# Kernel tuning notes

Hardware: AMD Instinct MI355X
Metric: run time of the kernel (lower is better)

Reference implementation:

```python
import jax, jax.numpy as jnp
import numpy as np

# --- hyperparameters (match init_kwargs / torch defaults) ---
BLOCK_SIZE = 11
MAX_DISP = 48
CONF_TH = 0.3
DS = 2
ALPHA = 0.85          # photometric SSIM weight
GT_TH = 2.0           # GT anchor threshold
SIGN_W, MAG_W = 0.3, 0.7
W_GT, W_PHOTO, W_SIGNMAG, W_SMOOTH = 1.0, 1.0, 0.5, 0.1


def _avg_pool(x, k, stride, pad):
    # torch F.avg_pool2d with count_include_pad=True (default): zero-padded sum / k^2
    s = jax.lax.reduce_window(x, 0.0, jax.lax.add, (1, 1, k, k), (1, 1, stride, stride),
                              ((0, 0), (0, 0), (pad, pad), (pad, pad)))
    return s / (k * k)


def _ssim(x, y):
    C1, C2 = 0.01 ** 2, 0.03 ** 2
    p = lambda t: _avg_pool(t, 3, 1, 1)
    mx, my = p(x), p(y)
    sx = jnp.maximum(p(x * x) - mx * mx, 0.0)
    sy = jnp.maximum(p(y * y) - my * my, 0.0)
    sxy = p(x * y) - mx * my
    n = (2 * mx * my + C1) * (2 * sxy + C2)
    d = (mx * mx + my * my + C1) * (sx + sy + C2)
    return jnp.clip((1 - n / d) / 2, 0.0, 1.0)


def _gt_anchor(pred, gt, conf, occ):
    pos = (gt > GT_TH).astype(pred.dtype)
    trust = conf * occ * pos
    return (trust * jnp.abs(pred - gt)).sum() / jnp.maximum(trust.sum(), 1.0)


def _photometric(disp, left, right):
    B, C, H, W = left.shape
    xb = jnp.arange(W, dtype=disp.dtype)[None, None, None, :]
    xs = xb - disp                                   # sampling x coord (grid_sample, align_corners=True)
    xc = jnp.clip(xs, 0.0, W - 1.0)                  # padding_mode='border'
    x0 = jnp.floor(xc)
    w = xc - x0
    x0i = x0.astype(jnp.int32)
    x1i = jnp.minimum(x0i + 1, W - 1)
    gather = lambda idx: jnp.take_along_axis(right, jnp.broadcast_to(idx, (B, C, H, W)), axis=3)
    warped = gather(x0i) * (1.0 - w) + gather(x1i) * w   # y grid is identity under align_corners
    valid = ((xs > 0) & (xs < W - 1)).astype(disp.dtype)
    l1 = jnp.abs(left - warped).mean(axis=1, keepdims=True)
    ss = _ssim(left, warped).mean(axis=1, keepdims=True)
    err = ALPHA * ss + (1.0 - ALPHA) * l1
    return (err * valid).sum() / jnp.maximum(valid.sum(), 1.0)


def _compute_ncc_disp(left, right):
    B, C, Ho, Wo = left.shape
    lg = _avg_pool(left, DS, DS, 0).mean(axis=1, keepdims=True)   # half-res grayscale
    rg = _avg_pool(right, DS, DS, 0).mean(axis=1, keepdims=True)
    H, W = lg.shape[2], lg.shape[3]
    md = MAX_DISP // DS
    bs, pad = BLOCK_SIZE, BLOCK_SIZE // 2
    p = lambda t: _avg_pool(t, bs, 1, pad)
    lm = p(lg)
    ls = jnp.sqrt(jnp.maximum(p(lg * lg) - lm * lm, 1e-8))
    best_c = jnp.full((B, 1, H, W), -1.0, dtype=jnp.float32)
    best_d = jnp.zeros((B, 1, H, W), dtype=jnp.float32)
    for d in range(-md, md + 1):          # fixed small set of shift offsets
        if d == 0:
            continue
        if d > 0:
            rs = jnp.pad(rg[:, :, :, d:], ((0, 0), (0, 0), (0, 0), (0, d)))
        else:
            rs = jnp.pad(rg[:, :, :, :W + d], ((0, 0), (0, 0), (0, 0), (-d, 0)))
        rm = p(rs)
        rstd = jnp.sqrt(jnp.maximum(p(rs * rs) - rm * rm, 1e-8))
        cross = p(lg * rs)
        ncc = (cross - lm * rm) / (ls * rstd + 1e-8)
        better = ncc > best_c
        best_c = jnp.where(better, ncc, best_c)
        best_d = jnp.where(better, jnp.float32(d), best_d)
    nd = best_d * float(DS)
    nc = jnp.maximum(best_c, 0.0)
    # nearest upsample back to full res (exact integer factor)
    nd = jnp.repeat(jnp.repeat(nd, DS, axis=2), DS, axis=3)
    nc = jnp.repeat(jnp.repeat(nc, DS, axis=2), DS, axis=3)
    nc = nc * (nc > CONF_TH).astype(nc.dtype)
    return jax.lax.stop_gradient(nd), jax.lax.stop_gradient(nc)   # torch @no_grad


def _sign_magnitude(pred, left, right):
    nd, nc = _compute_ncc_disp(left, right)
    active = (nc > 0).astype(pred.dtype)
    n = jnp.maximum(active.sum(), 1.0)
    sign_map = jnp.sign(nd) * active
    l_sign = (jnp.maximum(-pred * sign_map, 0.0) * active).sum() / n
    l_mag = (nc * jnp.abs(pred - nd) * active).sum() / n
    return SIGN_W * l_sign + MAG_W * l_mag


def _smoothness(disp, img):
    ddx = jnp.abs(disp[:, :, :, 1:] - disp[:, :, :, :-1])
    ddy = jnp.abs(disp[:, :, 1:, :] - disp[:, :, :-1, :])
    idx = jnp.abs(img[:, :, :, 1:] - img[:, :, :, :-1]).mean(axis=1, keepdims=True)
    idy = jnp.abs(img[:, :, 1:, :] - img[:, :, :-1, :]).mean(axis=1, keepdims=True)
    return (ddx * jnp.exp(-idx)).mean() + (ddy * jnp.exp(-idy)).mean()


def _total_loss(pred, gt, conf, occ, left, right):
    return (W_GT * _gt_anchor(pred, gt, conf, occ)
            + W_PHOTO * _photometric(pred, left, right)
            + W_SIGNMAG * _sign_magnitude(pred, left, right)
            + W_SMOOTH * _smoothness(pred, left))


def setup_inputs() -> dict:
    key = jax.random.key(0)
    k = jax.random.split(key, 6)
    B, H, W = 4, 544, 960
    return {
        "pred_disp": jax.random.normal(k[0], (B, 1, H, W), dtype=jnp.float32) * 8.0,
        "gt_disp": jax.random.uniform(k[1], (B, 1, H, W), dtype=jnp.float32) * 20.0,
        "gt_conf": jax.random.uniform(k[2], (B, 1, H, W), dtype=jnp.float32),
        "gt_occ": jax.random.uniform(k[3], (B, 1, H, W), dtype=jnp.float32),
        "left_img": jax.random.uniform(k[4], (B, 3, H, W), dtype=jnp.float32),
        "right_img": jax.random.uniform(k[5], (B, 3, H, W), dtype=jnp.float32),
    }


def reference(pred_disp, gt_disp, gt_conf, gt_occ, left_img, right_img):
    return _total_loss(pred_disp, gt_disp, gt_conf, gt_occ, left_img, right_img)
```

## Files before the change

kernel.cpp:

```cpp
#include <hip/hip_runtime.h>
#include <hip/hip_bf16.h>

constexpr int B  = 4;
constexpr int H  = 544;
constexpr int W  = 960;
constexpr int H2 = 272;
constexpr int W2 = 480;
constexpr int NH = B * H2 * W2;
constexpr int NF = B * H * W;

constexpr int TPW = 32, TPH = 8;
constexpr int SW = TPW + 2, SH = TPH + 2;
constexpr int NSTAGE = SW * SH;
constexpr int GX = W / TPW;
constexpr int GY = H / TPH;
constexpr int NBLK  = GX * GY * B;
constexpr int NBLK2 = (NH + 255) / 256;

__device__ inline float waveSum(float v) {
  #pragma unroll
  for (int off = 32; off > 0; off >>= 1) v += __shfl_down(v, off, 64);
  return v;
}

__global__ __launch_bounds__(256) void k_pix(const float* __restrict__ pred,
                                             const float* __restrict__ gt,
                                             const float* __restrict__ conf,
                                             const float* __restrict__ occ,
                                             const float* __restrict__ left,
                                             const float* __restrict__ right,
                                             float* __restrict__ lg,
                                             float* __restrict__ rg,
                                             float* __restrict__ partialsA) {
  const int bx = blockIdx.x % GX;
  const int by = (blockIdx.x / GX) % GY;
  const int b  = blockIdx.x / (GX * GY);
  const int x0 = bx * TPW, y0 = by * TPH;
  const int tid = threadIdx.x;

  const float* dispb = pred + (size_t)b * H * W;
  const float* lb = left  + (size_t)b * 3 * H * W;
  const float* rb = right + (size_t)b * 3 * H * W;

  __shared__ float4 L4s[NSTAGE];
  __shared__ float4 W4s[NSTAGE];

  for (int e = tid; e < NSTAGE; e += 256) {
    int r = e / SW, c = e % SW;
    int yy = y0 - 1 + r, xx = x0 - 1 + c;
    float4 l4 = make_float4(0.f, 0.f, 0.f, 0.f);
    float4 w4 = make_float4(0.f, 0.f, 0.f, 0.f);
    if (yy >= 0 && yy < H && xx >= 0 && xx < W) {
      float dv = dispb[yy * W + xx];
      float xsv = (float)xx - dv;
      float xc = fminf(fmaxf(xsv, 0.f), (float)(W - 1));
      float x0f = floorf(xc);
      float w = xc - x0f;
      int x0i = (int)x0f;
      int x1i = min(x0i + 1, W - 1);
      const float* l0 = lb + (size_t)yy * W;
      const float* r0 = rb + (size_t)yy * W;
      l4.x = l0[xx];
      l4.y = l0[(size_t)H * W + xx];
      l4.z = l0[2 * (size_t)H * W + xx];
      l4.w = dv;
      w4.x = r0[x0i] * (1.f - w) + r0[x1i] * w;
      w4.y = r0[(size_t)H * W + x0i] * (1.f - w) + r0[(size_t)H * W + x1i] * w;
      w4.z = r0[2 * (size_t)H * W + x0i] * (1.f - w) + r0[2 * (size_t)H * W + x1i] * w;
    }
    L4s[e] = l4; W4s[e] = w4;
  }
  __syncthreads();

  if (tid < 64) {
    int hx = tid & 15, hy = tid >> 4;
    int y2g = (y0 >> 1) + hy, x2g = (x0 >> 1) + hx;
    int i00 = (2 * hy + 1) * SW + (2 * hx + 1);
    float4 a00 = L4s[i00], a01 = L4s[i00 + 1], a10 = L4s[i00 + SW], a11 = L4s[i00 + SW + 1];
    float sl = 0.f;
    sl += a00.x + a01.x + a10.x + a11.x;
    sl += a00.y + a01.y + a10.y + a11.y;
    sl += a00.z + a01.z + a10.z + a11.z;
    float sr = 0.f;
    int yy2 = y0 + 2 * hy, xx2 = x0 + 2 * hx;
    #pragma unroll
    for (int c = 0; c < 3; c++) {
      const float* rp = rb + (size_t)(c * H + yy2) * W + xx2;
      sr += rp[0] + rp[1] + rp[W] + rp[W + 1];
    }
    size_t ho = (size_t)b * (H2 * W2) + (size_t)y2g * W2 + x2g;
    lg[ho] = sl * (1.f / 12.f);
    rg[ho] = sr * (1.f / 12.f);
  }

  float v[6];
  #pragma unroll
  for (int s = 0; s < 6; s++) v[s] = 0.f;

  {
    const int tx = tid & 31, ty = tid >> 5;
    const int x = x0 + tx, y = y0 + ty;
    const size_t gidx = (size_t)b * H * W + (size_t)y * W + x;
    const int ci = (ty + 1) * SW + (tx + 1);

    float sl[3] = {0,0,0}, sw[3] = {0,0,0}, sl2[3] = {0,0,0},
          sw2[3] = {0,0,0}, slw[3] = {0,0,0};
    float4 cl4, cw4, rl4, dl4;
    #pragma unroll
    for (int dy = -1; dy <= 1; dy++) {
      #pragma unroll
      for (int dx = -1; dx <= 1; dx++) {
        int ni = ci + dy * SW + dx;
        float4 a = L4s[ni];
        float4 wv = W4s[ni];
        sl[0] += a.x;  sl2[0] += a.x * a.x;  sw[0] += wv.x;  sw2[0] += wv.x * wv.x;  slw[0] += a.x * wv.x;
        sl[1] += a.y;  sl2[1] += a.y * a.y;  sw[1] += wv.y;  sw2[1] += wv.y * wv.y;  slw[1] += a.y * wv.y;
        sl[2] += a.z;  sl2[2] += a.z * a.z;  sw[2] += wv.z;  sw2[2] += wv.z * wv.z;  slw[2] += a.z * wv.z;
        if (dy == 0 && dx == 0) { cl4 = a; cw4 = wv; }
        if (dy == 0 && dx == 1) rl4 = a;
        if (dy == 1 && dx == 0) dl4 = a;
      }
    }
    float ds = cl4.w;

    {
      float g = gt[gidx];
      float trust = (g > 2.0f) ? conf[gidx] * occ[gidx] : 0.f;
      v[0] = trust * fabsf(ds - g);
      v[1] = trust;
    }

    {
      float xs = (float)x - ds;
      bool valid = (xs > 0.f) && (xs < (float)(W - 1));
      float cl[3] = {cl4.x, cl4.y, cl4.z};
      float cw[3] = {cw4.x, cw4.y, cw4.z};
      float ssm = 0.f, l1m = 0.f;
      #pragma unroll
      for (int c = 0; c < 3; c++) {
        float mx = sl[c] * (1.f / 9.f), my = sw[c] * (1.f / 9.f);
        float sx = fmaxf(sl2[c] * (1.f / 9.f) - mx * mx, 0.f);
        float sy = fmaxf(sw2[c] * (1.f / 9.f) - my * my, 0.f);
        float sxy = slw[c] * (1.f / 9.f) - mx * my;
        float n  = (2.f * mx * my + 1e-4f) * (2.f * sxy + 9e-4f);
        float dd = (mx * mx + my * my + 1e-4f) * (sx + sy + 9e-4f);
        float ss = (1.f - n / dd) * 0.5f;
        ss = fminf(fmaxf(ss, 0.f), 1.f);
        ssm += ss;
        l1m += fabsf(cl[c] - cw[c]);
      }
      ssm *= (1.f / 3.f); l1m *= (1.f / 3.f);
      float err = 0.85f * ssm + 0.15f * l1m;
      if (valid) { v[2] = err; v[3] = 1.f; }
    }

    if (x < W - 1) {
      float ddx = fabsf(rl4.w - ds);
      float idx = fabsf(rl4.x - cl4.x) + fabsf(rl4.y - cl4.y) + fabsf(rl4.z - cl4.z);
      v[4] = ddx * __expf(-idx * (1.f / 3.f));
    }
    if (y < H - 1) {
      float ddy = fabsf(dl4.w - ds);
      float idy = fabsf(dl4.x - cl4.x) + fabsf(dl4.y - cl4.y) + fabsf(dl4.z - cl4.z);
      v[5] = ddy * __expf(-idy * (1.f / 3.f));
    }
  }

  __shared__ float sm[4][6];
  int wave = threadIdx.x >> 6, lane = threadIdx.x & 63;
  #pragma unroll
  for (int s = 0; s < 6; s++) {
    float r = waveSum(v[s]);
    if (lane == 0) sm[wave][s] = r;
  }
  __syncthreads();
  if (threadIdx.x < 6) {
    float t = sm[0][threadIdx.x] + sm[1][threadIdx.x] +
              sm[2][threadIdx.x] + sm[3][threadIdx.x];
    partialsA[(size_t)threadIdx.x * NBLK + blockIdx.x] = t;
  }
}

__global__ __launch_bounds__(256) void k_ncc(const float* __restrict__ lg,
                                             const float* __restrict__ rg,
                                             float* __restrict__ bcA,
                                             float* __restrict__ bdA) {
  const int z = blockIdx.z;
  const int b = z >> 1, grp = z & 1;
  const int dmin = grp ? 1 : -24;
  const int x0 = blockIdx.x * 64;
  const int y0 = blockIdx.y * 8;
  const int tid = threadIdx.x;

  __shared__ __align__(16) float SM[5844];
  float* LGs = SM;
  float* RMS = SM;
  float* RGs = SM + 1392;
  float* POOL = SM + 3140;
  float* P1 = SM + 5444;
  float* P2 = SM + 5644;

  const float* lgb = lg + (size_t)b * (H2 * W2);
  const float* rgb = rg + (size_t)b * (H2 * W2);

  for (int e = tid; e < 18 * 74; e += 256) {
    int r = e / 74, c = e % 74;
    int gy = y0 - 5 + r, gxx = x0 - 5 + c;
    LGs[e] = (gy >= 0 && gy < H2 && gxx >= 0 && gxx < W2) ? lgb[gy * W2 + gxx] : 0.f;
  }
  const int col0RG = x0 - 5 + dmin;
  for (int e = tid; e < 18 * 97; e += 256) {
    int r = e / 97, c = e % 97;
    int gy = y0 - 5 + r, gxx = col0RG + c;
    RGs[e] = (gy >= 0 && gy < H2 && gxx >= 0 && gxx < W2) ? rgb[gy * W2 + gxx] : 0.f;
  }
  __syncthreads();

  const int hg = tid & 7, hr = tid >> 3;
  float lgc[18];
  float* LH1 = POOL;
  float* LH2 = POOL + 1152;
  if (hr < 18) {
    #pragma unroll
    for (int k = 0; k < 18; k++) lgc[k] = LGs[hr * 74 + 8 * hg + k];
    float w1[8], w2[8];
    float s1 = 0.f, s2 = 0.f;
    #pragma unroll
    for (int k = 0; k < 11; k++) { s1 += lgc[k]; s2 += lgc[k] * lgc[k]; }
    w1[0] = s1; w2[0] = s2;
    #pragma unroll
    for (int j = 1; j < 8; j++) {
      s1 += lgc[j + 10] - lgc[j - 1];
      s2 += lgc[j + 10] * lgc[j + 10] - lgc[j - 1] * lgc[j - 1];
      w1[j] = s1; w2[j] = s2;
    }
    *(float4*)&LH1[hr * 64 + 8 * hg]     = make_float4(w1[0], w1[1], w1[2], w1[3]);
    *(float4*)&LH1[hr * 64 + 8 * hg + 4] = make_float4(w1[4], w1[5], w1[6], w1[7]);
    *(float4*)&LH2[hr * 64 + 8 * hg]     = make_float4(w2[0], w2[1], w2[2], w2[3]);
    *(float4*)&LH2[hr * 64 + 8 * hg + 4] = make_float4(w2[4], w2[5], w2[6], w2[7]);
  }
  const bool headT = (grp == 1) && (x0 == 0);
  const bool tailT = (grp == 0) && (x0 == 448);
  if (headT || tailT) {
    int gcol0 = headT ? 0 : 456;
    for (int e = tid; e < 8 * 24; e += 256) {
      int y = e / 24, i = e % 24;
      int lc = gcol0 + i - col0RG;
      float v1 = 0.f, v2 = 0.f;
      if (lc >= 0 && lc < 97) {
        #pragma unroll
        for (int dy = 0; dy < 11; dy++) {
          float v = RGs[(y + dy) * 97 + lc];
          v1 += v; v2 += v * v;
        }
      }
      P1[y * 25 + i + 1] = v1;
      P2[y * 25 + i + 1] = v2;
    }
  }
  __syncthreads();

  if ((headT || tailT) && tid < 8) {
    int y = tid;
    float s1 = 0.f, s2 = 0.f;
    P1[y * 25] = 0.f; P2[y * 25] = 0.f;
    for (int k = 0; k < 24; k++) {
      s1 += P1[y * 25 + k + 1]; P1[y * 25 + k + 1] = s1;
      s2 += P2[y * 25 + k + 1]; P2[y * 25 + k + 1] = s2;
    }
  }
  const int vx = tid & 63;
  const int vys = (tid >> 6) * 2;
  float lmS[2], lsS[2];
  {
    float s1 = 0.f, s2 = 0.f;
    #pragma unroll
    for (int dy = 0; dy < 11; dy++) { s1 += LH1[(vys + dy) * 64 + vx]; s2 += LH2[(vys + dy) * 64 + vx]; }
    #pragma unroll
    for (int k = 0; k < 2; k++) {
      if (k) {
        s1 += LH1[(vys + k + 10) * 64 + vx] - LH1[(vys + k - 1) * 64 + vx];
        s2 += LH2[(vys + k + 10) * 64 + vx] - LH2[(vys + k - 1) * 64 + vx];
      }
      float m = s1 * (1.f / 121.f);
      float s = sqrtf(fmaxf(s2 * (1.f / 121.f) - m * m, 1e-8f));
      lmS[k] = m * 121.f;
      lsS[k] = s * 121.f;
    }
  }
  __syncthreads();

  float* VR1 = POOL;
  float* VR2 = POOL + 776;
  if (tid < 194) {
    int c = tid % 97;
    int rr0 = (tid / 97) * 4;
    float s1 = 0.f, s2 = 0.f;
    #pragma unroll
    for (int dy = 0; dy < 11; dy++) {
      float v = RGs[(rr0 + dy) * 97 + c];
      s1 += v; s2 += v * v;
    }
    VR1[rr0 * 97 + c] = s1; VR2[rr0 * 97 + c] = s2;
    #pragma unroll
    for (int k = 1; k < 4; k++) {
      float vin  = RGs[(rr0 + k + 10) * 97 + c];
      float vout = RGs[(rr0 + k - 1) * 97 + c];
      s1 += vin - vout;
      s2 += vin * vin - vout * vout;
      VR1[(rr0 + k) * 97 + c] = s1; VR2[(rr0 + k) * 97 + c] = s2;
    }
  }
  __syncthreads();

  {
    int r = tid >> 5, seg = tid & 31;
    int c0 = seg * 3;
    if (c0 < 87) {
      float s1 = 0.f, s2 = 0.f;
      #pragma unroll
      for (int m = 0; m < 11; m++) { s1 += VR1[r * 97 + c0 + m]; s2 += VR2[r * 97 + c0 + m]; }
      #pragma unroll
      for (int j = 0; j < 3; j++) {
        if (j) {
          s1 += VR1[r * 97 + c0 + j + 10] - VR1[r * 97 + c0 + j - 1];
          s2 += VR2[r * 97 + c0 + j + 10] - VR2[r * 97 + c0 + j - 1];
        }
        if (c0 + j < 87) {
          float rm = s1 * (1.f / 121.f);
          float rstd = sqrtf(fmaxf(s2 * (1.f / 121.f) - rm * rm, 1e-8f));
          *(float2*)&RMS[r * 174 + 2 * (c0 + j)] = make_float2(rm, rstd);
        }
      }
    }
  }
  __syncthreads();

  float* CH0 = POOL;
  float* CH1 = POOL + 1152;
  const int gx = x0 + vx;
  const bool headL = (grp == 1) && (gx < 5);
  const bool tailL = (grp == 0) && (gx > 474);
  const bool edgeL = headL || tailL;
  float bnum[2], bden[2], bdd[2];
  #pragma unroll
  for (int k = 0; k < 2; k++) { bnum[k] = -1.f; bden[k] = 1.f; bdd[k] = 0.f; }

  for (int it = 0; it < 12; ++it) {
    const int d0 = dmin + 2 * it;
    if (hr < 18) {
      const int c0 = 8 * hg + 2 * it;
      float rgv[19];
      #pragma unroll
      for (int j = 0; j < 19; j++) rgv[j] = RGs[hr * 97 + c0 + j];
      float ca[8], cb[8];
      float sa = 0.f, sb = 0.f;
      #pragma unroll
      for (int k = 0; k < 11; k++) { sa += lgc[k] * rgv[k]; sb += lgc[k] * rgv[k + 1]; }
      ca[0] = sa; cb[0] = sb;
      #pragma unroll
      for (int j = 1; j < 8; j++) {
        sa += lgc[j + 10] * rgv[j + 10] - lgc[j - 1] * rgv[j - 1];
        sb += lgc[j + 10] * rgv[j + 11] - lgc[j - 1] * rgv[j];
        ca[j] = sa; cb[j] = sb;
      }
      *(float4*)&CH0[hr * 64 + 8 * hg]     = make_float4(ca[0], ca[1], ca[2], ca[3]);
      *(float4*)&CH0[hr * 64 + 8 * hg + 4] = make_float4(ca[4], ca[5], ca[6], ca[7]);
      *(float4*)&CH1[hr * 64 + 8 * hg]     = make_float4(cb[0], cb[1], cb[2], cb[3]);
      *(float4*)&CH1[hr * 64 + 8 * hg + 4] = make_float4(cb[4], cb[5], cb[6], cb[7]);
    }
    __syncthreads();
    {
      float a0 = 0.f, a1 = 0.f;
      #pragma unroll
      for (int dy = 0; dy < 11; dy++) { a0 += CH0[(vys + dy) * 64 + vx]; a1 += CH1[(vys + dy) * 64 + vx]; }
      #pragma unroll
      for (int k = 0; k < 2; k++) {
        if (k) {
          a0 += CH0[(vys + k + 10) * 64 + vx] - CH0[(vys + k - 1) * 64 + vx];
          a1 += CH1[(vys + k + 10) * 64 + vx] - CH1[(vys + k - 1) * 64 + vx];
        }
        #pragma unroll
        for (int h = 0; h < 2; h++) {
          int d = d0 + h;
          float cs = h ? a1 : a0;
          int rvi = vx + 2 * it + h;
          float2 ms = *(const float2*)&RMS[(vys + k) * 174 + 2 * rvi];
          float rm = ms.x, rstd = ms.y;
          if (edgeL) {
            float rs = rm * 121.f;
            float r2 = (rstd * rstd + rm * rm) * 121.f;
            int a, bI;
            if (headL) { a = max(gx - 5 + d, 0); bI = d; }
            else       { a = 24 + d; bI = min(gx + 5 + d, 479) - 455; }
            rs -= P1[(vys + k) * 25 + bI] - P1[(vys + k) * 25 + a];
            r2 -= P2[(vys + k) * 25 + bI] - P2[(vys + k) * 25 + a];
            rm = rs * (1.f / 121.f);
            rstd = sqrtf(fmaxf(r2 * (1.f / 121.f) - rm * rm, 1e-8f));
          }
          float num = __builtin_fmaf(-lmS[k], rm, cs);
          float den = __builtin_fmaf(lsS[k], rstd, 1.21e-6f);
          if (num * bden[k] > bnum[k] * den) { bnum[k] = num; bden[k] = den; bdd[k] = (float)d; }
        }
      }
    }
    __syncthreads();
  }

  if (gx < W2) {
    float* bcp = bcA + (size_t)grp * NH + (size_t)b * (H2 * W2);
    float* bdp = bdA + (size_t)grp * NH + (size_t)b * (H2 * W2);
    #pragma unroll
    for (int k = 0; k < 2; k++) {
      size_t o = (size_t)(y0 + vys + k) * W2 + gx;
      bcp[o] = bnum[k] / bden[k];
      bdp[o] = bdd[k];
    }
  }
}

__global__ __launch_bounds__(256) void k_sgm(const float* __restrict__ pred,
                                             const float* __restrict__ bcA,
                                             const float* __restrict__ bdA,
                                             float* __restrict__ partialsB) {
  int tid = blockIdx.x * 256 + threadIdx.x;
  float v6 = 0.f, v7 = 0.f, v8 = 0.f;
  if (tid < NH) {
    int b = tid / (H2 * W2);
    int rem = tid % (H2 * W2);
    int y2 = rem / W2, x2 = rem % W2;
    float bcv = bcA[tid];
    float bdv = bdA[tid];
    {
      float c = bcA[(size_t)NH + tid];
      if (c > bcv) { bcv = c; bdv = bdA[(size_t)NH + tid]; }
    }
    if (bcv > 0.3f) {
      float nd = bdv * 2.f;
      float sgn = (nd > 0.f) ? 1.f : ((nd < 0.f) ? -1.f : 0.f);
      const float* pb = pred + (size_t)b * H * W;
      #pragma unroll
      for (int dy = 0; dy < 2; dy++) {
        #pragma unroll
        for (int dx = 0; dx < 2; dx++) {
          float p = pb[(size_t)(2 * y2 + dy) * W + 2 * x2 + dx];
          v6 += fmaxf(-p * sgn, 0.f);
          v7 += bcv * fabsf(p - nd);
        }
      }
      v8 = 4.f;
    }
  }
  __shared__ float sm[4][3];
  int wave = threadIdx.x >> 6, lane = threadIdx.x & 63;
  float r;
  r = waveSum(v6); if (lane == 0) sm[wave][0] = r;
  r = waveSum(v7); if (lane == 0) sm[wave][1] = r;
  r = waveSum(v8); if (lane == 0) sm[wave][2] = r;
  __syncthreads();
  if (threadIdx.x < 3) {
    float t = sm[0][threadIdx.x] + sm[1][threadIdx.x] +
              sm[2][threadIdx.x] + sm[3][threadIdx.x];
    partialsB[(size_t)threadIdx.x * NBLK2 + blockIdx.x] = t;
  }
}

__global__ __launch_bounds__(1024) void k_final(const float* __restrict__ PA,
                                                const float* __restrict__ PB,
                                                float* __restrict__ out) {
  __shared__ float red[9][16];
  int lane = threadIdx.x & 63, wave = threadIdx.x >> 6;
  #pragma unroll
  for (int s = 0; s < 6; s++) {
    float l = 0.f;
    for (int i = threadIdx.x; i < NBLK; i += 1024) l += PA[(size_t)s * NBLK + i];
    l = waveSum(l);
    if (lane == 0) red[s][wave] = l;
  }
  #pragma unroll
  for (int s = 0; s < 3; s++) {
    float l = 0.f;
    for (int i = threadIdx.x; i < NBLK2; i += 1024) l += PB[(size_t)s * NBLK2 + i];
    l = waveSum(l);
    if (lane == 0) red[6 + s][wave] = l;
  }
  __syncthreads();
  if (threadIdx.x == 0) {
    float a[9];
    #pragma unroll
    for (int s = 0; s < 9; s++) {
      float t = 0.f;
      #pragma unroll
      for (int q = 0; q < 16; q++) t += red[s][q];
      a[s] = t;
    }
    float gtl = a[0] / fmaxf(a[1], 1.f);
    float ph  = a[2] / fmaxf(a[3], 1.f);
    float n   = fmaxf(a[8], 1.f);
    float smv = 0.3f * (a[6] / n) + 0.7f * (a[7] / n);
    float smo = a[4] * (1.f / ((float)B * H * (W - 1)))
              + a[5] * (1.f / ((float)B * (H - 1) * W));
    out[0] = gtl + ph + 0.5f * smv + 0.1f * smo;
  }
}

extern "C" void kernel_launch(void* const* d_in, const int* in_sizes, int n_in,
                              void* d_out, int out_size, void* d_ws, size_t ws_size,
                              hipStream_t stream) {
  const float* pred  = (const float*)d_in[0];
  const float* gt    = (const float*)d_in[1];
  const float* conf  = (const float*)d_in[2];
  const float* occ   = (const float*)d_in[3];
  const float* left  = (const float*)d_in[4];
  const float* right = (const float*)d_in[5];
  float* out = (float*)d_out;

  float* ws = (float*)d_ws;
  float* lg  = ws;
  float* rg  = ws + (size_t)NH;
  float* bcA = ws + 2 * (size_t)NH;
  float* bdA = ws + 4 * (size_t)NH;
  float* partialsA = ws + 6 * (size_t)NH;
  float* partialsB = partialsA + 6 * (size_t)NBLK;

  k_pix<<<NBLK, 256, 0, stream>>>(pred, gt, conf, occ, left, right,
                                  lg, rg, partialsA);

  dim3 nccGrid(8, 34, 8);
  k_ncc<<<nccGrid, 256, 0, stream>>>(lg, rg, bcA, bdA);

  k_sgm<<<NBLK2, 256, 0, stream>>>(pred, bcA, bdA, partialsB);

  k_final<<<1, 1024, 0, stream>>>(partialsA, partialsB, out);
}
```

Before: 233.0 us.

## Merge NCC disparity halves into one block and fuse sign-magnitude reduction

Each NCC block now sweeps all 48 disparities instead of splitting negative and positive ranges across two blocks. It keeps the best correlation in registers and evaluates the sign/magnitude terms directly against pred. This removes the bcA/bdA workspace round trip and the separate k_sgm launch, and it avoids loading the overlapping left tile and reduction setup twice. In exchange the grid is halved to 1088 blocks, each running twice as many iterations with slightly more shared memory, which lowers parallelism and occupancy.

```diff
diff --git a/kernel.cpp b/kernel.cpp
--- a/kernel.cpp
+++ b/kernel.cpp
@@ -15,7 +15,7 @@
 constexpr int GX = W / TPW;
 constexpr int GY = H / TPH;
 constexpr int NBLK  = GX * GY * B;
-constexpr int NBLK2 = (NH + 255) / 256;
+constexpr int NBLK3 = 8 * 34 * B;
 
 __device__ inline float waveSum(float v) {
   #pragma unroll
@@ -183,22 +183,20 @@
 
 __global__ __launch_bounds__(256) void k_ncc(const float* __restrict__ lg,
                                              const float* __restrict__ rg,
-                                             float* __restrict__ bcA,
-                                             float* __restrict__ bdA) {
-  const int z = blockIdx.z;
-  const int b = z >> 1, grp = z & 1;
-  const int dmin = grp ? 1 : -24;
+                                             const float* __restrict__ pred,
+                                             float* __restrict__ partialsB) {
+  const int b = blockIdx.z;
   const int x0 = blockIdx.x * 64;
   const int y0 = blockIdx.y * 8;
   const int tid = threadIdx.x;
 
-  __shared__ __align__(16) float SM[5844];
+  __shared__ __align__(16) float SM[6692];
   float* LGs = SM;
   float* RMS = SM;
-  float* RGs = SM + 1392;
-  float* POOL = SM + 3140;
-  float* P1 = SM + 5444;
-  float* P2 = SM + 5644;
+  float* RGs = SM + 1792;
+  float* POOL = SM + 3988;
+  float* P1 = SM + 6292;
+  float* P2 = SM + 6492;
 
   const float* lgb = lg + (size_t)b * (H2 * W2);
   const float* rgb = rg + (size_t)b * (H2 * W2);
@@ -208,9 +206,9 @@
     int gy = y0 - 5 + r, gxx = x0 - 5 + c;
     LGs[e] = (gy >= 0 && gy < H2 && gxx >= 0 && gxx < W2) ? lgb[gy * W2 + gxx] : 0.f;
   }
-  const int col0RG = x0 - 5 + dmin;
-  for (int e = tid; e < 18 * 97; e += 256) {
-    int r = e / 97, c = e % 97;
+  const int col0RG = x0 - 29;
+  for (int e = tid; e < 18 * 122; e += 256) {
+    int r = e / 122, c = e % 122;
     int gy = y0 - 5 + r, gxx = col0RG + c;
     RGs[e] = (gy >= 0 && gy < H2 && gxx >= 0 && gxx < W2) ? rgb[gy * W2 + gxx] : 0.f;
   }
@@ -239,18 +237,18 @@
     *(float4*)&LH2[hr * 64 + 8 * hg]     = make_float4(w2[0], w2[1], w2[2], w2[3]);
     *(float4*)&LH2[hr * 64 + 8 * hg + 4] = make_float4(w2[4], w2[5], w2[6], w2[7]);
   }
-  const bool headT = (grp == 1) && (x0 == 0);
-  const bool tailT = (grp == 0) && (x0 == 448);
+  const bool headT = (x0 == 0);
+  const bool tailT = (x0 == 448);
   if (headT || tailT) {
     int gcol0 = headT ? 0 : 456;
     for (int e = tid; e < 8 * 24; e += 256) {
       int y = e / 24, i = e % 24;
       int lc = gcol0 + i - col0RG;
       float v1 = 0.f, v2 = 0.f;
-      if (lc >= 0 && lc < 97) {
+      if (lc >= 0 && lc < 122) {
         #pragma unroll
         for (int dy = 0; dy < 11; dy++) {
-          float v = RGs[(y + dy) * 97 + lc];
+          float v = RGs[(y + dy) * 122 + lc];
           v1 += v; v2 += v * v;
         }
       }
@@ -291,46 +289,44 @@
   __syncthreads();
 
   float* VR1 = POOL;
-  float* VR2 = POOL + 776;
-  if (tid < 194) {
-    int c = tid % 97;
-    int rr0 = (tid / 97) * 4;
+  float* VR2 = POOL + 976;
+  if (tid < 244) {
+    int c = tid % 122;
+    int rr0 = (tid / 122) * 4;
     float s1 = 0.f, s2 = 0.f;
     #pragma unroll
     for (int dy = 0; dy < 11; dy++) {
-      float v = RGs[(rr0 + dy) * 97 + c];
+      float v = RGs[(rr0 + dy) * 122 + c];
       s1 += v; s2 += v * v;
     }
-    VR1[rr0 * 97 + c] = s1; VR2[rr0 * 97 + c] = s2;
+    VR1[rr0 * 122 + c] = s1; VR2[rr0 * 122 + c] = s2;
     #pragma unroll
     for (int k = 1; k < 4; k++) {
-      float vin  = RGs[(rr0 + k + 10) * 97 + c];
-      float vout = RGs[(rr0 + k - 1) * 97 + c];
+      float vin  = RGs[(rr0 + k + 10) * 122 + c];
+      float vout = RGs[(rr0 + k - 1) * 122 + c];
       s1 += vin - vout;
       s2 += vin * vin - vout * vout;
-      VR1[(rr0 + k) * 97 + c] = s1; VR2[(rr0 + k) * 97 + c] = s2;
+      VR1[(rr0 + k) * 122 + c] = s1; VR2[(rr0 + k) * 122 + c] = s2;
     }
   }
   __syncthreads();
 
   {
     int r = tid >> 5, seg = tid & 31;
-    int c0 = seg * 3;
-    if (c0 < 87) {
+    int c0 = seg * 4;
+    if (c0 < 112) {
       float s1 = 0.f, s2 = 0.f;
       #pragma unroll
-      for (int m = 0; m < 11; m++) { s1 += VR1[r * 97 + c0 + m]; s2 += VR2[r * 97 + c0 + m]; }
-      #pragma unroll
-      for (int j = 0; j < 3; j++) {
+      for (int m = 0; m < 11; m++) { s1 += VR1[r * 122 + c0 + m]; s2 += VR2[r * 122 + c0 + m]; }
+      #pragma unroll
+      for (int j = 0; j < 4; j++) {
         if (j) {
-          s1 += VR1[r * 97 + c0 + j + 10] - VR1[r * 97 + c0 + j - 1];
-          s2 += VR2[r * 97 + c0 + j + 10] - VR2[r * 97 + c0 + j - 1];
+          s1 += VR1[r * 122 + c0 + j + 10] - VR1[r * 122 + c0 + j - 1];
+          s2 += VR2[r * 122 + c0 + j + 10] - VR2[r * 122 + c0 + j - 1];
         }
-        if (c0 + j < 87) {
-          float rm = s1 * (1.f / 121.f);
-          float rstd = sqrtf(fmaxf(s2 * (1.f / 121.f) - rm * rm, 1e-8f));
-          *(float2*)&RMS[r * 174 + 2 * (c0 + j)] = make_float2(rm, rstd);
-        }
+        float rm = s1 * (1.f / 121.f);
+        float rstd = sqrtf(fmaxf(s2 * (1.f / 121.f) - rm * rm, 1e-8f));
+        *(float2*)&RMS[r * 224 + 2 * (c0 + j)] = make_float2(rm, rstd);
       }
     }
   }
@@ -339,20 +335,17 @@
   float* CH0 = POOL;
   float* CH1 = POOL + 1152;
   const int gx = x0 + vx;
-  const bool headL = (grp == 1) && (gx < 5);
-  const bool tailL = (grp == 0) && (gx > 474);
-  const bool edgeL = headL || tailL;
   float bnum[2], bden[2], bdd[2];
   #pragma unroll
   for (int k = 0; k < 2; k++) { bnum[k] = -1.f; bden[k] = 1.f; bdd[k] = 0.f; }
 
-  for (int it = 0; it < 12; ++it) {
-    const int d0 = dmin + 2 * it;
+  for (int it = 0; it < 24; ++it) {
+    const int d0 = (it < 12) ? (2 * it - 24) : (2 * it - 23);
     if (hr < 18) {
-      const int c0 = 8 * hg + 2 * it;
+      const int c0 = 8 * hg + d0 + 24;
       float rgv[19];
       #pragma unroll
-      for (int j = 0; j < 19; j++) rgv[j] = RGs[hr * 97 + c0 + j];
+      for (int j = 0; j < 19; j++) rgv[j] = RGs[hr * 122 + c0 + j];
       float ca[8], cb[8];
       float sa = 0.f, sb = 0.f;
       #pragma unroll
@@ -384,14 +377,15 @@
         for (int h = 0; h < 2; h++) {
           int d = d0 + h;
           float cs = h ? a1 : a0;
-          int rvi = vx + 2 * it + h;
-          float2 ms = *(const float2*)&RMS[(vys + k) * 174 + 2 * rvi];
+          int rvi = vx + d + 24;
+          float2 ms = *(const float2*)&RMS[(vys + k) * 224 + 2 * rvi];
           float rm = ms.x, rstd = ms.y;
-          if (edgeL) {
+          bool eh = (d > 0) ? (gx < 5) : (gx > 474);
+          if (eh) {
             float rs = rm * 121.f;
             float r2 = (rstd * rstd + rm * rm) * 121.f;
             int a, bI;
-            if (headL) { a = max(gx - 5 + d, 0); bI = d; }
+            if (d > 0) { a = max(gx - 5 + d, 0); bI = d; }
             else       { a = 24 + d; bI = min(gx + 5 + d, 479) - 455; }
             rs -= P1[(vys + k) * 25 + bI] - P1[(vys + k) * 25 + a];
             r2 -= P2[(vys + k) * 25 + bI] - P2[(vys + k) * 25 + a];
@@ -407,61 +401,38 @@
     __syncthreads();
   }
 
+  float v6 = 0.f, v7 = 0.f, v8 = 0.f;
   if (gx < W2) {
-    float* bcp = bcA + (size_t)grp * NH + (size_t)b * (H2 * W2);
-    float* bdp = bdA + (size_t)grp * NH + (size_t)b * (H2 * W2);
+    const float* pb = pred + (size_t)b * H * W;
     #pragma unroll
     for (int k = 0; k < 2; k++) {
-      size_t o = (size_t)(y0 + vys + k) * W2 + gx;
-      bcp[o] = bnum[k] / bden[k];
-      bdp[o] = bdd[k];
-    }
-  }
-}
-
-__global__ __launch_bounds__(256) void k_sgm(const float* __restrict__ pred,
-                                             const float* __restrict__ bcA,
-                                             const float* __restrict__ bdA,
-                                             float* __restrict__ partialsB) {
-  int tid = blockIdx.x * 256 + threadIdx.x;
-  float v6 = 0.f, v7 = 0.f, v8 = 0.f;
-  if (tid < NH) {
-    int b = tid / (H2 * W2);
-    int rem = tid % (H2 * W2);
-    int y2 = rem / W2, x2 = rem % W2;
-    float bcv = bcA[tid];
-    float bdv = bdA[tid];
-    {
-      float c = bcA[(size_t)NH + tid];
-      if (c > bcv) { bcv = c; bdv = bdA[(size_t)NH + tid]; }
-    }
-    if (bcv > 0.3f) {
-      float nd = bdv * 2.f;
-      float sgn = (nd > 0.f) ? 1.f : ((nd < 0.f) ? -1.f : 0.f);
-      const float* pb = pred + (size_t)b * H * W;
-      #pragma unroll
-      for (int dy = 0; dy < 2; dy++) {
-        #pragma unroll
-        for (int dx = 0; dx < 2; dx++) {
-          float p = pb[(size_t)(2 * y2 + dy) * W + 2 * x2 + dx];
-          v6 += fmaxf(-p * sgn, 0.f);
-          v7 += bcv * fabsf(p - nd);
-        }
-      }
-      v8 = 4.f;
-    }
-  }
-  __shared__ float sm[4][3];
-  int wave = threadIdx.x >> 6, lane = threadIdx.x & 63;
+      float bc = bnum[k] / bden[k];
+      if (bc > 0.3f) {
+        float nd = bdd[k] * 2.f;
+        float sgn = (nd > 0.f) ? 1.f : ((nd < 0.f) ? -1.f : 0.f);
+        const float* p0 = pb + (size_t)(2 * (y0 + vys + k)) * W + 2 * gx;
+        float p00 = p0[0], p01 = p0[1];
+        float p10 = p0[W], p11 = p0[W + 1];
+        v6 += fmaxf(-p00 * sgn, 0.f) + fmaxf(-p01 * sgn, 0.f)
+            + fmaxf(-p10 * sgn, 0.f) + fmaxf(-p11 * sgn, 0.f);
+        v7 += bc * (fabsf(p00 - nd) + fabsf(p01 - nd)
+                  + fabsf(p10 - nd) + fabsf(p11 - nd));
+        v8 += 4.f;
+      }
+    }
+  }
+  float* red = P1;
+  int wave = tid >> 6, lane = tid & 63;
   float r;
-  r = waveSum(v6); if (lane == 0) sm[wave][0] = r;
-  r = waveSum(v7); if (lane == 0) sm[wave][1] = r;
-  r = waveSum(v8); if (lane == 0) sm[wave][2] = r;
-  __syncthreads();
-  if (threadIdx.x < 3) {
-    float t = sm[0][threadIdx.x] + sm[1][threadIdx.x] +
-              sm[2][threadIdx.x] + sm[3][threadIdx.x];
-    partialsB[(size_t)threadIdx.x * NBLK2 + blockIdx.x] = t;
+  r = waveSum(v6); if (lane == 0) red[wave * 3 + 0] = r;
+  r = waveSum(v7); if (lane == 0) red[wave * 3 + 1] = r;
+  r = waveSum(v8); if (lane == 0) red[wave * 3 + 2] = r;
+  __syncthreads();
+  if (tid < 3) {
+    float t = red[0 * 3 + tid] + red[1 * 3 + tid] +
+              red[2 * 3 + tid] + red[3 * 3 + tid];
+    int bid = ((int)blockIdx.z * 34 + (int)blockIdx.y) * 8 + (int)blockIdx.x;
+    partialsB[(size_t)tid * NBLK3 + bid] = t;
   }
 }
 
@@ -480,7 +451,7 @@
   #pragma unroll
   for (int s = 0; s < 3; s++) {
     float l = 0.f;
-    for (int i = threadIdx.x; i < NBLK2; i += 1024) l += PB[(size_t)s * NBLK2 + i];
+    for (int i = threadIdx.x; i < NBLK3; i += 1024) l += PB[(size_t)s * NBLK3 + i];
     l = waveSum(l);
     if (lane == 0) red[6 + s][wave] = l;
   }
@@ -518,18 +489,14 @@
   float* ws = (float*)d_ws;
   float* lg  = ws;
   float* rg  = ws + (size_t)NH;
-  float* bcA = ws + 2 * (size_t)NH;
-  float* bdA = ws + 4 * (size_t)NH;
-  float* partialsA = ws + 6 * (size_t)NH;
+  float* partialsA = ws + 2 * (size_t)NH;
   float* partialsB = partialsA + 6 * (size_t)NBLK;
 
   k_pix<<<NBLK, 256, 0, stream>>>(pred, gt, conf, occ, left, right,
                                   lg, rg, partialsA);
 
-  dim3 nccGrid(8, 34, 8);
-  k_ncc<<<nccGrid, 256, 0, stream>>>(lg, rg, bcA, bdA);
-
-  k_sgm<<<NBLK2, 256, 0, stream>>>(pred, bcA, bdA, partialsB);
+  dim3 nccGrid(8, 34, B);
+  k_ncc<<<nccGrid, 256, 0, stream>>>(lg, rg, pred, partialsB);
 
   k_final<<<1, 1024, 0, stream>>>(partialsA, partialsB, out);
 }
```

Result: faster. 227.4 us (-2.4%).
